# Kernel optimization log

Hardware: AMD Instinct MI355X
Metric: run time of the kernel (lower is better)

The kernel has to match this reference:

```python
import jax, jax.numpy as jnp
import numpy as np

S = 768          # size2d (dense splat grid side)
D1 = 3           # lattice dimension d1 == d == 3 in the module

_ELEVATE = jnp.asarray(
    np.array([[2, -1, -1], [-1, 2, -1], [-1, -1, 2]], dtype=np.float32)
    / np.float32(np.sqrt(6.0)))
# canonical: arange(3) rows, then canonical[-i:, i] = i - 3 for i in 1..2
_CANONICAL = jnp.array([[0, 1, 2], [0, 1, -1], [0, -2, -1]], dtype=jnp.int32)


def _keys_and_barycentric(pc):
    # pc: (B, 3, N) float32
    B, _, N = pc.shape
    elevated = jnp.einsum('ij,bjn->bin', _ELEVATE, pc)          # (B,3,N)
    greedy = jnp.round(elevated / D1) * D1                       # (B,3,N)
    emg = elevated - greedy
    order = jnp.argsort(-emg, axis=1)                            # descending sort indices
    rank = jnp.argsort(order, axis=1)                            # inverse permutation = rank of each dim
    rs = jnp.sum(greedy, axis=1, keepdims=True) / D1             # remainder_sum (B,1,N)
    rf = rank.astype(jnp.float32)
    cond = (((rf >= D1 - rs) & (rs > 0)).astype(jnp.float32)
            + ((rf < -rs) & (rs < 0)).astype(jnp.float32))
    sign = -(rs > 0).astype(jnp.float32) + (rs < 0).astype(jnp.float32)
    greedy = greedy + D1 * sign * cond
    rank = rank + (D1 * sign * cond).astype(rank.dtype) + rs.astype(jnp.int32)
    emg = elevated - greedy
    gl = greedy.astype(jnp.int32)
    bi = jnp.arange(B)[:, None, None]
    pi = jnp.arange(N)[None, None, :]
    bary = jnp.zeros((B, D1 + 1, N), jnp.float32)
    # note: self.d == self.d1 == 3 in the source, so both scatters hit the
    # same index (indices unique per scatter -> exact cancellation, faithful)
    bary = bary.at[bi, D1 - rank, pi].add(emg)
    bary = bary.at[bi, D1 - rank, pi].add(-emg)
    bary = bary / D1
    bary = bary.at[:, 0, :].add(1.0 + bary[:, D1, :])
    bary = bary[:, :D1, :]                                       # (B,3,N)
    keys = gl[:, :, :, None] + _CANONICAL[rank]                  # (B,3,N,3)
    return keys, bary


def setup_inputs() -> dict:
    key = jax.random.key(0)
    k1, k2 = jax.random.split(key)
    B, N = 32, 16384
    # scale 50 spreads lattice keys over a few hundred cells, in-bounds for S=768
    pc1 = jax.random.normal(k1, (B, 3, N), dtype=jnp.float32) * 50.0
    features = jax.random.normal(k2, (B, 3, N), dtype=jnp.float32)
    return {"pc1": pc1, "features": features}


def reference(pc1, features):
    keys, bary = _keys_and_barycentric(pc1)
    B, _, N = features.shape
    d = 2
    coord = keys[:, :d].reshape(B, d, D1 * N)                    # (B,2,3N)
    offset = coord.min(axis=2)                                   # (B,2)
    coord = coord - offset[:, :, None]
    # tmp[b,c,v,n] = bary[b,v,n] * features[b,c,n] -> flatten (n,v) -> (B,3N,3)
    tmp = bary[:, None, :, :] * features[:, :, None, :]          # (B,3,3,N)
    tmp = tmp.transpose(0, 1, 3, 2).reshape(B, 3, D1 * N).transpose(0, 2, 1)
    bidx = jnp.arange(B)[:, None]
    splat = jnp.zeros((B, S, S, 3), jnp.float32).at[
        bidx, coord[:, 0], coord[:, 1]].add(tmp)                 # dense scatter-add
    pick = (-offset) % D1                                        # (B,2)
    g = S // D1
    rows = pick[:, 0:1] + D1 * jnp.arange(g)[None, :]            # (B,g)
    cols = pick[:, 1:2] + D1 * jnp.arange(g)[None, :]
    filt = splat[jnp.arange(B)[:, None, None], rows[:, :, None], cols[:, None, :]]
    return (filt, filt)
```

## Files before the change

### kernel.cpp

```cpp
#include <hip/hip_runtime.h>


#define GV 256
#define NB 16384
#define BB 32
#define TR 4
#define NSLOT 128
#define NJ (GV / TR + 1)
#define TILE_FLOATS (TR * GV * 3)
#define ROWF4 (GV * 3 / 4)
#define CAPLOG 11
#define NEGB 0x40000000
#define PPT 4

typedef float vfloat4 __attribute__((ext_vector_type(4)));

__device__ __forceinline__ void lattice_point(const float* __restrict__ pc,
                                              long base, int n,
                                              int& k0o, int& k1o, int& r0o, int& r1o) {
#pragma clang fp contract(off)
  const float S6 = 2.449489742783178f;
  const float CA = 2.0f / S6;
  const float CB = -1.0f / S6;

  float p0 = pc[base + 0 * (long)NB + n];
  float p1 = pc[base + 1 * (long)NB + n];
  float p2 = pc[base + 2 * (long)NB + n];

  float e0 = CA * p0 + CB * p1 + CB * p2;
  float e1 = CB * p0 + CA * p1 + CB * p2;
  float e2 = CB * p0 + CB * p1 + CA * p2;

  float q0 = rintf(e0 / 3.0f);
  float q1 = rintf(e1 / 3.0f);
  float q2 = rintf(e2 / 3.0f);
  int k0 = (int)q0, k1 = (int)q1, k2 = (int)q2;

  float m0 = e0 - q0 * 3.0f;
  float m1 = e1 - q1 * 3.0f;
  float m2 = e2 - q2 * 3.0f;

  int rank0 = (m1 > m0) + (m2 > m0);
  int rank1 = (m0 > m1) + (m2 > m1) + (m0 == m1);
  int rs = k0 + k1 + k2;

  if (rs > 0) {
    int t = 3 - rs;
    if (rank0 >= t) { k0 -= 1; rank0 -= 3; }
    if (rank1 >= t) { k1 -= 1; rank1 -= 3; }
  } else if (rs < 0) {
    int t = -rs;
    if (rank0 < t) { k0 += 1; rank0 += 3; }
    if (rank1 < t) { k1 += 1; rank1 += 3; }
  }
  rank0 += rs; rank1 += rs;

  k0o = k0; k1o = k1; r0o = rank0; r1o = rank1;
}

__device__ __forceinline__ int k_shift(int off) {
  int pick = ((-off) % 3 + 3) % 3;
  return (off + pick) / 3;
}

__device__ __forceinline__ unsigned int bf16_rne(float f) {
  unsigned int u = __float_as_uint(f);
  return (u + 0x7FFFu + ((u >> 16) & 1u)) >> 16;
}

__global__ void __launch_bounds__(256) prep_kernel(const float* __restrict__ pc,
                                                   const float* __restrict__ feat,
                                                   unsigned int* __restrict__ offs,
                                                   unsigned int* __restrict__ gcount,
                                                   uint2* __restrict__ buckets) {
  int i = blockIdx.x;
  int b = (i & 7) + 8 * ((i >> 3) & 3);
  int chunk = i >> 5;
  int n0 = chunk * 1024 + threadIdx.x;

  __shared__ unsigned int cnt[NSLOT], basev[NSLOT];
  __shared__ int s0w[4], s1w[4];
  if (threadIdx.x < NSLOT) cnt[threadIdx.x] = 0;
  __syncthreads();

  long pcB = (long)b * 3 * NB;
  int mloc0 = 0x7FFFFFFF, mloc1 = 0x7FFFFFFF;
  int mslot[PPT];
  unsigned int sl[PPT];
  uint2 ent[PPT];

#pragma unroll
  for (int p = 0; p < PPT; ++p) {
    int n = n0 + p * 256;
    int k0, k1, r0, r1;
    lattice_point(pc, pcB, n, k0, k1, r0, r1);

    int kb = k0 + 8192;
    int m = (kb >> 2) & (NSLOT - 1);

    long fbB = pcB + n;
    unsigned int b0 = bf16_rne(feat[fbB]);
    unsigned int b1 = bf16_rne(feat[fbB + NB]);
    unsigned int b2 = bf16_rne(feat[fbB + 2 * NB]);
    ent[p].x = (unsigned int)(kb & 3) | ((unsigned int)(k1 + 512) << 2) | (b0 << 13);
    ent[p].y = b1 | (b2 << 16);

    mslot[p] = m;
    sl[p] = atomicAdd(&cnt[m], 1u);

    mloc0 = min(mloc0, 3 * k0 - r0);
    mloc1 = min(mloc1, 3 * k1 - r1);
  }

  for (int off = 32; off > 0; off >>= 1) {
    mloc0 = min(mloc0, __shfl_down(mloc0, off));
    mloc1 = min(mloc1, __shfl_down(mloc1, off));
  }
  int lane = threadIdx.x & 63, wv = threadIdx.x >> 6;
  if (lane == 0) { s0w[wv] = mloc0; s1w[wv] = mloc1; }
  __syncthreads();
  if (threadIdx.x == 0) {
    int a = min(min(s0w[0], s0w[1]), min(s0w[2], s0w[3]));
    int c = min(min(s1w[0], s1w[1]), min(s1w[2], s1w[3]));
    atomicMax(&offs[2 * b + 0], (unsigned int)(NEGB - a));
    atomicMax(&offs[2 * b + 1], (unsigned int)(NEGB - c));
  }
  if (threadIdx.x < NSLOT && cnt[threadIdx.x] != 0)
    basev[threadIdx.x] = atomicAdd(&gcount[b * NSLOT + threadIdx.x], cnt[threadIdx.x]);
  __syncthreads();

#pragma unroll
  for (int p = 0; p < PPT; ++p) {
    int m = mslot[p];
    buckets[(((long)b * NSLOT + m) << CAPLOG) + basev[m] + sl[p]] = ent[p];
  }
}

__global__ void __launch_bounds__(256) tile_kernel(const unsigned int* __restrict__ offs,
                                                   const unsigned int* __restrict__ gcount,
                                                   const uint2* __restrict__ buckets,
                                                   float* __restrict__ out, long half) {
  __shared__ float hist[TILE_FLOATS];

  int i = blockIdx.x;
  int w = i & 31;
  int b = (w & 7) + 8 * ((w >> 3) & 3);
  int j = i >> 5;

  for (int t = threadIdx.x; t < TILE_FLOATS; t += 256) hist[t] = 0.0f;

  int off0 = NEGB - (int)offs[2 * b + 0];
  int off1 = NEGB - (int)offs[2 * b + 1];
  int s0b = k_shift(off0) + 8192;
  int s1b = k_shift(off1) + 512;
  int kt = (s0b >> 2) + j;
  int m = kt & (NSLOT - 1);
  int rlo = 4 * kt - s0b;

  unsigned int count = gcount[b * NSLOT + m];
  const uint2* bk = buckets + (((long)b * NSLOT + m) << CAPLOG);
  __syncthreads();

  for (unsigned int t = threadIdx.x; t < count; t += 256) {
    uint2 e = bk[t];
    int rr = e.x & 3;
    int cc = (int)((e.x >> 2) & 1023) - s1b;
    if (cc < GV) {
      float f0 = __uint_as_float((e.x >> 13) << 16);
      float f1 = __uint_as_float(e.y << 16);
      float f2 = __uint_as_float(e.y & 0xFFFF0000u);
      int hbase = (rr * GV + cc) * 3;
      atomicAdd(&hist[hbase + 0], f0);
      atomicAdd(&hist[hbase + 1], f1);
      atomicAdd(&hist[hbase + 2], f2);
    }
  }
  __syncthreads();

  const vfloat4* hs = reinterpret_cast<const vfloat4*>(hist);
  for (int t = threadIdx.x; t < TR * ROWF4; t += 256) {
    int rr = t / ROWF4;
    int col = t - rr * ROWF4;
    int orow = rlo + rr;
    if ((unsigned)orow < GV) {
      vfloat4 v = hs[t];
      long g = (((long)b * GV + orow) * GV * 3) + col * 4;
      __builtin_nontemporal_store(v, reinterpret_cast<vfloat4*>(out + g));
      __builtin_nontemporal_store(v, reinterpret_cast<vfloat4*>(out + half + g));
    }
  }
}

extern "C" void kernel_launch(void* const* d_in, const int* in_sizes, int n_in,
                              void* d_out, int out_size, void* d_ws, size_t ws_size,
                              hipStream_t stream) {
  const float* pc = (const float*)d_in[0];
  const float* feat = (const float*)d_in[1];
  float* out = (float*)d_out;

  char* ws = (char*)d_ws;
  unsigned int* offs = (unsigned int*)ws;
  unsigned int* gcount = (unsigned int*)(ws + 256);
  uint2* buckets = (uint2*)(ws + 32768);

  const long half = (long)BB * GV * GV * 3;

  hipMemsetAsync(ws, 0, 32768, stream);

  prep_kernel<<<dim3(BB * (NB / 1024)), dim3(256), 0, stream>>>(pc, feat, offs, gcount, buckets);
  tile_kernel<<<dim3(BB * NJ), dim3(256), 0, stream>>>(offs, gcount, buckets, out, half);
}
```

Baseline: 93.56 us.

## Replace global atomics and memset with per-chunk buckets and prefix sums

The prep kernel now writes each chunk's entries into a private per-chunk, per-slot region of fixed capacity and stores per-chunk counts and minima without global atomics. The tile kernel reduces the chunk minima and builds a prefix sum over chunk counts to walk the sub-buckets. This removes the hipMemsetAsync launch and the global atomicMax/atomicAdd traffic. In exchange it adds a serial prefix scan, a linear chunk search per element, and a fixed capacity of 384 per chunk-slot that could overflow on skewed inputs.

```diff
diff --git a/kernel.cpp b/kernel.cpp
--- a/kernel.cpp
+++ b/kernel.cpp
@@ -6,11 +6,11 @@
 #define BB 32
 #define TR 4
 #define NSLOT 128
+#define NCH 16
 #define NJ (GV / TR + 1)
 #define TILE_FLOATS (TR * GV * 3)
 #define ROWF4 (GV * 3 / 4)
-#define CAPLOG 11
-#define NEGB 0x40000000
+#define CAP 384
 #define PPT 4
 
 typedef float vfloat4 __attribute__((ext_vector_type(4)));
@@ -70,24 +70,22 @@
 
 __global__ void __launch_bounds__(256) prep_kernel(const float* __restrict__ pc,
                                                    const float* __restrict__ feat,
-                                                   unsigned int* __restrict__ offs,
-                                                   unsigned int* __restrict__ gcount,
+                                                   int* __restrict__ mins,
+                                                   int* __restrict__ cntArr,
                                                    uint2* __restrict__ buckets) {
   int i = blockIdx.x;
   int b = (i & 7) + 8 * ((i >> 3) & 3);
   int chunk = i >> 5;
   int n0 = chunk * 1024 + threadIdx.x;
 
-  __shared__ unsigned int cnt[NSLOT], basev[NSLOT];
+  __shared__ unsigned int cnt[NSLOT];
   __shared__ int s0w[4], s1w[4];
   if (threadIdx.x < NSLOT) cnt[threadIdx.x] = 0;
   __syncthreads();
 
   long pcB = (long)b * 3 * NB;
+  long bktB = ((long)b * NSLOT * NCH + chunk) * CAP;
   int mloc0 = 0x7FFFFFFF, mloc1 = 0x7FFFFFFF;
-  int mslot[PPT];
-  unsigned int sl[PPT];
-  uint2 ent[PPT];
 
 #pragma unroll
   for (int p = 0; p < PPT; ++p) {
@@ -102,11 +100,12 @@
     unsigned int b0 = bf16_rne(feat[fbB]);
     unsigned int b1 = bf16_rne(feat[fbB + NB]);
     unsigned int b2 = bf16_rne(feat[fbB + 2 * NB]);
-    ent[p].x = (unsigned int)(kb & 3) | ((unsigned int)(k1 + 512) << 2) | (b0 << 13);
-    ent[p].y = b1 | (b2 << 16);
-
-    mslot[p] = m;
-    sl[p] = atomicAdd(&cnt[m], 1u);
+    uint2 ent;
+    ent.x = (unsigned int)(kb & 3) | ((unsigned int)(k1 + 512) << 2) | (b0 << 13);
+    ent.y = b1 | (b2 << 16);
+
+    unsigned int sl = atomicAdd(&cnt[m], 1u);
+    buckets[bktB + (long)m * (NCH * CAP) + sl] = ent;
 
     mloc0 = min(mloc0, 3 * k0 - r0);
     mloc1 = min(mloc1, 3 * k1 - r1);
@@ -120,49 +119,57 @@
   if (lane == 0) { s0w[wv] = mloc0; s1w[wv] = mloc1; }
   __syncthreads();
   if (threadIdx.x == 0) {
-    int a = min(min(s0w[0], s0w[1]), min(s0w[2], s0w[3]));
-    int c = min(min(s1w[0], s1w[1]), min(s1w[2], s1w[3]));
-    atomicMax(&offs[2 * b + 0], (unsigned int)(NEGB - a));
-    atomicMax(&offs[2 * b + 1], (unsigned int)(NEGB - c));
-  }
-  if (threadIdx.x < NSLOT && cnt[threadIdx.x] != 0)
-    basev[threadIdx.x] = atomicAdd(&gcount[b * NSLOT + threadIdx.x], cnt[threadIdx.x]);
-  __syncthreads();
-
-#pragma unroll
-  for (int p = 0; p < PPT; ++p) {
-    int m = mslot[p];
-    buckets[(((long)b * NSLOT + m) << CAPLOG) + basev[m] + sl[p]] = ent[p];
-  }
-}
-
-__global__ void __launch_bounds__(256) tile_kernel(const unsigned int* __restrict__ offs,
-                                                   const unsigned int* __restrict__ gcount,
+    mins[(b * NCH + chunk) * 2 + 0] = min(min(s0w[0], s0w[1]), min(s0w[2], s0w[3]));
+    mins[(b * NCH + chunk) * 2 + 1] = min(min(s1w[0], s1w[1]), min(s1w[2], s1w[3]));
+  }
+  if (threadIdx.x < NSLOT)
+    cntArr[(b * NCH + chunk) * NSLOT + threadIdx.x] = (int)cnt[threadIdx.x];
+}
+
+__global__ void __launch_bounds__(256) tile_kernel(const int* __restrict__ mins,
+                                                   const int* __restrict__ cntArr,
                                                    const uint2* __restrict__ buckets,
                                                    float* __restrict__ out, long half) {
   __shared__ float hist[TILE_FLOATS];
+  __shared__ int sOff[2];
+  __shared__ int pre[NCH + 1];
 
   int i = blockIdx.x;
   int w = i & 31;
   int b = (w & 7) + 8 * ((w >> 3) & 3);
   int j = i >> 5;
 
+  if (threadIdx.x < 2) {
+    int mn = 0x7FFFFFFF;
+#pragma unroll
+    for (int c = 0; c < NCH; ++c)
+      mn = min(mn, mins[(b * NCH + c) * 2 + threadIdx.x]);
+    sOff[threadIdx.x] = mn;
+  }
   for (int t = threadIdx.x; t < TILE_FLOATS; t += 256) hist[t] = 0.0f;
-
-  int off0 = NEGB - (int)offs[2 * b + 0];
-  int off1 = NEGB - (int)offs[2 * b + 1];
-  int s0b = k_shift(off0) + 8192;
-  int s1b = k_shift(off1) + 512;
+  __syncthreads();
+
+  int s0b = k_shift(sOff[0]) + 8192;
+  int s1b = k_shift(sOff[1]) + 512;
   int kt = (s0b >> 2) + j;
   int m = kt & (NSLOT - 1);
   int rlo = 4 * kt - s0b;
 
-  unsigned int count = gcount[b * NSLOT + m];
-  const uint2* bk = buckets + (((long)b * NSLOT + m) << CAPLOG);
-  __syncthreads();
-
-  for (unsigned int t = threadIdx.x; t < count; t += 256) {
-    uint2 e = bk[t];
+  if (threadIdx.x < NCH)
+    pre[threadIdx.x + 1] = cntArr[(b * NCH + threadIdx.x) * NSLOT + m];
+  __syncthreads();
+  if (threadIdx.x == 0) {
+    pre[0] = 0;
+    for (int c = 0; c < NCH; ++c) pre[c + 1] += pre[c];
+  }
+  __syncthreads();
+
+  int T = pre[NCH];
+  long base = ((long)b * NSLOT + m) * (NCH * CAP);
+  for (int t = threadIdx.x; t < T; t += 256) {
+    int c = 0;
+    while (pre[c + 1] <= t) ++c;
+    uint2 e = buckets[base + c * CAP + (t - pre[c])];
     int rr = e.x & 3;
     int cc = (int)((e.x >> 2) & 1023) - s1b;
     if (cc < GV) {
@@ -199,14 +206,12 @@
   float* out = (float*)d_out;
 
   char* ws = (char*)d_ws;
-  unsigned int* offs = (unsigned int*)ws;
-  unsigned int* gcount = (unsigned int*)(ws + 256);
-  uint2* buckets = (uint2*)(ws + 32768);
+  int* cntArr = (int*)ws;
+  int* mins = (int*)(ws + 262144);
+  uint2* buckets = (uint2*)(ws + 266240);
 
   const long half = (long)BB * GV * GV * 3;
 
-  hipMemsetAsync(ws, 0, 32768, stream);
-
-  prep_kernel<<<dim3(BB * (NB / 1024)), dim3(256), 0, stream>>>(pc, feat, offs, gcount, buckets);
-  tile_kernel<<<dim3(BB * NJ), dim3(256), 0, stream>>>(offs, gcount, buckets, out, half);
-}
+  prep_kernel<<<dim3(BB * NCH), dim3(256), 0, stream>>>(pc, feat, mins, cntArr, buckets);
+  tile_kernel<<<dim3(BB * NJ), dim3(256), 0, stream>>>(mins, cntArr, buckets, out, half);
+}
```

After: 92.74 us. No clear change (-0.9%).
